# Kernel optimization log

Measured on AMD Instinct MI355X. Metric: run time of the kernel, lower is better.

## Reference

```python
import jax, jax.numpy as jnp
import numpy as np

NUM_USERS = 1000000
NUM_ITEMS = 500000
NUM_R = 5
D = 64
B = 512
N = 30


def _mlp3(x, W1, b1, W2, b2, W3, b3):
    # Linear->ReLU->Linear->ReLU->Linear (as in MLP module)
    h = jax.nn.relu(x @ W1 + b1)
    h = jax.nn.relu(h @ W2 + b2)
    return h @ W3 + b3


def _attn(self_rep, neighs, W1, b1, W2, b2):
    # pi_rep = self_rep.unsqueeze(1).expand_as(neighs)
    rep = jnp.broadcast_to(jnp.expand_dims(self_rep, 1), neighs.shape)
    h = jax.nn.relu(jnp.concatenate([rep, neighs], -1) @ W1 + b1)
    s = h @ W2 + b2
    # NOTE: original torch code uses F.softmax(..., dim=0) (over the batch axis); kept faithfully
    return jax.nn.softmax(s, axis=0)


def _forward(fl, nodes_u, nodes_i, u_items_list, u_users_list, i_users_list,
             u_items_r, u_users_items, u_users_items_r, i_users_r):
    (E_u, E_i, E_r,
     gv_W1, gv_b1, gv_W2, gv_b2, gv_W3, gv_b3,
     attI_W1, attI_b1, attI_W2, attI_b2,
     attO_W1, attO_b1, attO_W2, attO_b2,
     attS_W1, attS_b1, attS_W2, attS_b2,
     atti_W1, atti_b1, atti_W2, atti_b2,
     linI_W, linI_b, linO_W, linO_b,
     umlp_W1, umlp_b1, umlp_W2, umlp_b2, umlp_W3, umlp_b3,
     gu_W1, gu_b1, gu_W2, gu_b2, gu_W3, gu_b3,
     ilin_W, ilin_b,
     g_W1, g_b1, g_W2, g_b2, g_W3, g_b3) = fl

    # ----- UserModeling: item-space aggregation -----
    pi = E_u[nodes_u]                                   # [B, d]
    er = E_r[u_items_r]                                 # [B, N, d]
    qa = E_i[u_items_list]                              # [B, N, d]
    xia = _mlp3(jnp.concatenate([qa, er], -1), gv_W1, gv_b1, gv_W2, gv_b2, gv_W3, gv_b3)
    alpha_ia = _attn(pi, xia, attI_W1, attI_b1, attI_W2, attI_b2)   # [B, N, 1]
    hi_I = jax.nn.relu(jnp.sum(alpha_ia * xia, 1) @ linI_W + linI_b)  # [B, d]

    # ----- UserModeling: social-space aggregation -----
    po = E_u[u_users_list]                              # [B, N, d]
    ero = E_r[u_users_items_r]                          # [B, N, N, d]
    qao = E_i[u_users_items]                            # [B, N, N, d]
    xoa = _mlp3(jnp.concatenate([qao, ero], -1), gv_W1, gv_b1, gv_W2, gv_b2, gv_W3, gv_b3)
    alpha_oa = _attn(po, xoa, attO_W1, attO_b1, attO_W2, attO_b2)   # [B, N, N, 1]
    ho_I = jax.nn.relu(jnp.sum(alpha_oa * xoa, 1) @ linO_W + linO_b)  # [B, N, d]
    # original att_S(ho_I, pi) does not shape-check; intended semantics: pi is self, ho_I are neighbors
    beta_io = _attn(pi, ho_I, attS_W1, attS_b1, attS_W2, attS_b2)   # [B, N, 1]
    hi_S = jax.nn.relu(jnp.sum(beta_io * ho_I, 1) @ linO_W + linO_b)  # original reuses linO (linS unused)
    hi = _mlp3(jnp.concatenate([hi_I, hi_S], -1), umlp_W1, umlp_b1, umlp_W2, umlp_b2, umlp_W3, umlp_b3)

    # ----- ItemModeling -----
    qj = E_i[nodes_i]                                   # [B, d]
    pt = E_u[i_users_list]                              # [B, N, d]
    er2 = E_r[i_users_r]                                # [B, N, d]
    fjt = _mlp3(jnp.concatenate([pt, er2], -1), gu_W1, gu_b1, gu_W2, gu_b2, gu_W3, gu_b3)
    mu_jt = _attn(qj, fjt, atti_W1, atti_b1, atti_W2, atti_b2)      # [B, N, 1]
    zj = jax.nn.relu(jnp.sum(mu_jt * fjt, 1) @ ilin_W + ilin_b)     # [B, d]

    # ----- Rating prediction -----
    gl = _mlp3(jnp.concatenate([hi, zj], -1), g_W1, g_b1, g_W2, g_b2, g_W3, g_b3)  # [B, 1]
    return gl


def setup_inputs() -> dict:
    key = jax.random.key(0)
    ks = iter(jax.random.split(key, 80))
    def P(*shape):
        return jax.random.normal(next(ks), shape, jnp.float32) * 0.05
    def I(shape, hi):
        return jax.random.randint(next(ks), shape, 0, hi, dtype=jnp.int32)
    d = D
    inp = {}
    inp['E_u'] = P(NUM_USERS, d)
    inp['E_i'] = P(NUM_ITEMS, d)
    inp['E_r'] = P(NUM_R, d)
    for pre in ['gv', 'umlp', 'gu']:
        inp[pre + '_W1'] = P(2 * d, d); inp[pre + '_b1'] = P(d)
        inp[pre + '_W2'] = P(d, d);     inp[pre + '_b2'] = P(d)
        inp[pre + '_W3'] = P(d, d);     inp[pre + '_b3'] = P(d)
    for pre in ['attI', 'attO', 'attS', 'atti']:
        inp[pre + '_W1'] = P(2 * d, d); inp[pre + '_b1'] = P(d)
        inp[pre + '_W2'] = P(d, 1);     inp[pre + '_b2'] = P(1)
    inp['linI_W'] = P(d, d); inp['linI_b'] = P(d)
    inp['linO_W'] = P(d, d); inp['linO_b'] = P(d)
    inp['ilin_W'] = P(d, d); inp['ilin_b'] = P(d)
    inp['g_W1'] = P(2 * d, 1); inp['g_b1'] = P(1)
    inp['g_W2'] = P(1, 1);     inp['g_b2'] = P(1)
    inp['g_W3'] = P(1, 1);     inp['g_b3'] = P(1)
    inp['nodes_u'] = I((B,), NUM_USERS)
    inp['nodes_i'] = I((B,), NUM_ITEMS)
    inp['u_items_list'] = I((B, N), NUM_ITEMS)
    inp['u_users_list'] = I((B, N), NUM_USERS)
    inp['i_users_list'] = I((B, N), NUM_USERS)
    inp['u_items_r'] = I((B, N), NUM_R)
    inp['u_users_items'] = I((B, N, N), NUM_ITEMS)
    inp['u_users_items_r'] = I((B, N, N), NUM_R)
    inp['i_users_r'] = I((B, N), NUM_R)
    return inp


def reference(E_u, E_i, E_r,
              gv_W1, gv_b1, gv_W2, gv_b2, gv_W3, gv_b3,
              attI_W1, attI_b1, attI_W2, attI_b2,
              attO_W1, attO_b1, attO_W2, attO_b2,
              attS_W1, attS_b1, attS_W2, attS_b2,
              atti_W1, atti_b1, atti_W2, atti_b2,
              linI_W, linI_b, linO_W, linO_b,
              umlp_W1, umlp_b1, umlp_W2, umlp_b2, umlp_W3, umlp_b3,
              gu_W1, gu_b1, gu_W2, gu_b2, gu_W3, gu_b3,
              ilin_W, ilin_b,
              g_W1, g_b1, g_W2, g_b2, g_W3, g_b3,
              nodes_u, nodes_i, u_items_list, u_users_list, i_users_list,
              u_items_r, u_users_items, u_users_items_r, i_users_r):
    fl = (E_u, E_i, E_r,
          gv_W1, gv_b1, gv_W2, gv_b2, gv_W3, gv_b3,
          attI_W1, attI_b1, attI_W2, attI_b2,
          attO_W1, attO_b1, attO_W2, attO_b2,
          attS_W1, attS_b1, attS_W2, attS_b2,
          atti_W1, atti_b1, atti_W2, atti_b2,
          linI_W, linI_b, linO_W, linO_b,
          umlp_W1, umlp_b1, umlp_W2, umlp_b2, umlp_W3, umlp_b3,
          gu_W1, gu_b1, gu_W2, gu_b2, gu_W3, gu_b3,
          ilin_W, ilin_b,
          g_W1, g_b1, g_W2, g_b2, g_W3, g_b3)
    return _forward(fl, nodes_u, nodes_i, u_items_list, u_users_list, i_users_list,
                    u_items_r, u_users_items, u_users_items_r, i_users_r)
```

## Files before the change

### kernel.cpp

```cpp
#include <hip/hip_runtime.h>
#include <cstdint>
#include <cstddef>


#define GB 512
#define GN 30
#define GD 64
#define IDX16(l) ((((l) & 15) << 2) | ((l) >> 4))

typedef unsigned short u16;
typedef __attribute__((ext_vector_type(8))) short short8v;
typedef __attribute__((ext_vector_type(4))) float f32x4;

__device__ __forceinline__ u16 f2bf(float x) {
  union { float f; uint32_t u; } c; c.f = x;
  uint32_t r = c.u + 0x7fffu + ((c.u >> 16) & 1u);
  return (u16)(r >> 16);
}
__device__ __forceinline__ float bf2f(u16 b) {
  union { float f; uint32_t u; } c; c.u = ((uint32_t)b) << 16; return c.f;
}
__device__ __forceinline__ float wave_sum(float v) {
#pragma unroll
  for (int off = 32; off >= 1; off >>= 1) v += __shfl_xor(v, off, 64);
  return v;
}

__global__ __launch_bounds__(256) void k_setup(
    const float* __restrict__ gvW1, const float* __restrict__ gvW2, const float* __restrict__ gvW3,
    const float* __restrict__ guW1, const float* __restrict__ guW2, const float* __restrict__ guW3,
    const float* __restrict__ umW1, const float* __restrict__ umW2, const float* __restrict__ umW3,
    const float* __restrict__ aOW1, const float* __restrict__ aIW1, const float* __restrict__ aiW1,
    const float* __restrict__ aSW1,
    const float* __restrict__ E_u, const float* __restrict__ E_i,
    const int* __restrict__ nodes_u, const int* __restrict__ nodes_i, const int* __restrict__ u_users,
    u16* gv1t, u16* gv2t, u16* gv3t, u16* gu1t, u16* gu2t, u16* gu3t,
    u16* um1t, u16* um2t, u16* um3t, u16* aOt, u16* aIt, u16* ait,
    float* piWI, float* piWS, float* qjWi, float* poW) {
  __shared__ float ws[64 * 64];
  int blk = blockIdx.x, t = threadIdx.x;
  if (blk < 240) {
    int o = blk * 256 + t;
    const float* src; u16* dst; int kind;
    if      (o < 8192)  {            src = gvW1; dst = gv1t; kind = 0; }
    else if (o < 12288) { o -= 8192;  src = gvW2; dst = gv2t; kind = 1; }
    else if (o < 16384) { o -= 12288; src = gvW3; dst = gv3t; kind = 1; }
    else if (o < 20480) { o -= 16384; src = aOW1; dst = aOt;  kind = 2; }
    else if (o < 28672) { o -= 20480; src = guW1; dst = gu1t; kind = 0; }
    else if (o < 32768) { o -= 28672; src = guW2; dst = gu2t; kind = 1; }
    else if (o < 36864) { o -= 32768; src = guW3; dst = gu3t; kind = 1; }
    else if (o < 40960) { o -= 36864; src = aIW1; dst = aIt;  kind = 2; }
    else if (o < 45056) { o -= 40960; src = aiW1; dst = ait;  kind = 2; }
    else if (o < 53248) { o -= 45056; src = umW1; dst = um1t; kind = 0; }
    else if (o < 57344) { o -= 53248; src = umW2; dst = um2t; kind = 1; }
    else                { o -= 57344; src = umW3; dst = um3t; kind = 1; }
    if (kind == 0) { int n = o >> 7, k = o & 127; dst[n * 128 + k] = f2bf(src[(size_t)k * 64 + n]); }
    else { int n = o >> 6, p = o & 63; int k = ((p & 3) << 4) | (p >> 2); if (kind == 2) k += 64;
           dst[n * 64 + p] = f2bf(src[(size_t)k * 64 + n]); }
    return;
  }
  int rb = blk - 240;
  const float* tab; const int* idx; const float* W; float* out; int base;
  if (rb < 16)      { tab = E_u; idx = nodes_u; W = aIW1; out = piWI; base = rb * 32; }
  else if (rb < 32) { tab = E_u; idx = nodes_u; W = aSW1; out = piWS; base = (rb - 16) * 32; }
  else if (rb < 48) { tab = E_i; idx = nodes_i; W = aiW1; out = qjWi; base = (rb - 32) * 32; }
  else              { tab = E_u; idx = u_users; W = aOW1; out = poW;  base = (rb - 48) * 32; }
  for (int i = t; i < 4096; i += 256) ws[i] = W[i];
  __syncthreads();
  int lane = t & 63, wave = t >> 6;
  int b0 = base + wave * 8;
  const float* p[8]; float acc[8];
#pragma unroll
  for (int r = 0; r < 8; r++) {
    p[r] = tab + (size_t)__builtin_amdgcn_readfirstlane(idx[b0 + r]) * 64;
    acc[r] = 0.f;
  }
#pragma unroll 8
  for (int k = 0; k < 64; k++) {
    float w = ws[k * 64 + lane];
#pragma unroll
    for (int r = 0; r < 8; r++) acc[r] = fmaf(p[r][k], w, acc[r]);
  }
#pragma unroll
  for (int r = 0; r < 8; r++) out[(size_t)(b0 + r) * 64 + lane] = acc[r];
}

__global__ __launch_bounds__(256, 2) void k_engine(
    const float* __restrict__ E_i, const float* __restrict__ E_r, const float* __restrict__ E_u,
    const int* __restrict__ uu_items, const int* __restrict__ uu_items_r,
    const int* __restrict__ u_items, const int* __restrict__ u_items_r,
    const int* __restrict__ i_users, const int* __restrict__ i_users_r,
    const u16* __restrict__ gv1t, const u16* __restrict__ gv2t, const u16* __restrict__ gv3t,
    const u16* __restrict__ gu1t, const u16* __restrict__ gu2t, const u16* __restrict__ gu3t,
    const float* __restrict__ gvb1, const float* __restrict__ gvb2, const float* __restrict__ gvb3,
    const float* __restrict__ gub1, const float* __restrict__ gub2, const float* __restrict__ gub3,
    const u16* __restrict__ aOt, const u16* __restrict__ aIt, const u16* __restrict__ ait,
    const float* __restrict__ aOb1, const float* __restrict__ aIb1, const float* __restrict__ aib1,
    const float* __restrict__ aOW2, const float* __restrict__ aIW2, const float* __restrict__ aiW2,
    const float* __restrict__ aOb2, const float* __restrict__ aIb2, const float* __restrict__ aib2,
    const float* __restrict__ poW, const float* __restrict__ piWI, const float* __restrict__ qjWi,
    u16* __restrict__ xoa_bf, u16* __restrict__ xia_bf, u16* __restrict__ fjt_bf,
    float* __restrict__ sOT, float* __restrict__ sIT, float* __restrict__ siT) {
  __shared__ __align__(16) u16 xs[64 * 136], w1s[64 * 136], hs[64 * 72];
  __shared__ float b1s[64], b2s[64], b3s[64], ab1s[64], aw2s[64];
  int t = threadIdx.x, blk = blockIdx.x;
  const float *tabA, *tabB, *selfW, *b1, *b2, *b3, *ab1, *aW2, *ab2p;
  const int *idxA, *idxB; const u16 *w1t, *w2t, *w3t, *att;
  u16* outB; float* sT; int tile0, modeNN;
  if (blk < 480) {
    tabA = E_i; idxA = uu_items; tabB = E_r; idxB = uu_items_r;
    w1t = gv1t; w2t = gv2t; w3t = gv3t; b1 = gvb1; b2 = gvb2; b3 = gvb3;
    att = aOt; ab1 = aOb1; aW2 = aOW2; ab2p = aOb2; selfW = poW;
    outB = xoa_bf; sT = sOT; tile0 = blk * 15; modeNN = 1;
  } else if (blk < 496) {
    int lb = blk - 480;
    tabA = E_i; idxA = u_items; tabB = E_r; idxB = u_items_r;
    w1t = gv1t; w2t = gv2t; w3t = gv3t; b1 = gvb1; b2 = gvb2; b3 = gvb3;
    att = aIt; ab1 = aIb1; aW2 = aIW2; ab2p = aIb2; selfW = piWI;
    outB = xia_bf; sT = sIT; tile0 = lb * 15; modeNN = 0;
  } else {
    int lb = blk - 496;
    tabA = E_u; idxA = i_users; tabB = E_r; idxB = i_users_r;
    w1t = gu1t; w2t = gu2t; w3t = gu3t; b1 = gub1; b2 = gub2; b3 = gub3;
    att = ait; ab1 = aib1; aW2 = aiW2; ab2p = aib2; selfW = qjWi;
    outB = fjt_bf; sT = siT; tile0 = lb * 15; modeNN = 0;
  }
  const int nt = 15;
  for (int i = t; i < 64 * 16; i += 256) { int n = i >> 4, j = i & 15;
    ((uint4*)(w1s + n * 136))[j] = ((const uint4*)(w1t + n * 128))[j]; }
  if (t < 64) { b1s[t] = b1[t]; b2s[t] = b2[t]; b3s[t] = b3[t];
                ab1s[t] = ab1[t]; aw2s[t] = aW2[t]; }
  __syncthreads();
  const int lane = t & 63, wave = t >> 6, m = lane & 15, quad = lane >> 4;
  const int lr = t >> 2, q = t & 3;
  short8v w2f[8], w3f[8], waf[8];
#pragma unroll
  for (int c = 0; c < 4; c++)
#pragma unroll
    for (int kk = 0; kk < 2; kk++) {
      int off = (c * 16 + m) * 64 + kk * 32 + quad * 8;
      w2f[c * 2 + kk] = *(const short8v*)(w2t + off);
      w3f[c * 2 + kk] = *(const short8v*)(w3t + off);
      waf[c * 2 + kk] = *(const short8v*)(att + off);
    }
  const float ab2v = ab2p[0];
  const f32x4 zz = {0.f, 0.f, 0.f, 0.f};
  float4 fr[8];
  {
    int row = tile0 * 64 + lr;
    const float* src = (q < 2) ? (tabA + (size_t)idxA[row] * 64 + q * 32)
                               : (tabB + (size_t)idxB[row] * 64 + (q - 2) * 32);
#pragma unroll
    for (int h = 0; h < 8; h++) fr[h] = ((const float4*)src)[h];
  }
  for (int it = 0; it < nt; it++) {
    int base = (tile0 + it) * 64;
    { u16* dst = xs + lr * 136 + q * 32;
#pragma unroll
      for (int h = 0; h < 8; h++) { float4 v = fr[h]; ushort4 u;
        u.x = f2bf(v.x); u.y = f2bf(v.y); u.z = f2bf(v.z); u.w = f2bf(v.w);
        *(ushort4*)(dst + h * 4) = u; } }
    if (it + 1 < nt) {
      int row = base + 64 + lr;
      const float* src = (q < 2) ? (tabA + (size_t)idxA[row] * 64 + q * 32)
                                 : (tabB + (size_t)idxB[row] * 64 + (q - 2) * 32);
#pragma unroll
      for (int h = 0; h < 8; h++) fr[h] = ((const float4*)src)[h];
    }
    f32x4 cc[4];
#pragma unroll
    for (int c = 0; c < 4; c++) cc[c] = zz;
#pragma unroll
    for (int kk = 0; kk < 4; kk++) {
      short8v av = *(const short8v*)(xs + (wave * 16 + m) * 136 + kk * 32 + quad * 8);
#pragma unroll
      for (int c = 0; c < 4; c++) {
        short8v bv = *(const short8v*)(w1s + (c * 16 + m) * 136 + kk * 32 + quad * 8);
        cc[c] = __builtin_amdgcn_mfma_f32_16x16x32_bf16(av, bv, cc[c], 0, 0, 0);
      }
    }
#pragma unroll
    for (int r = 0; r < 4; r++) { ushort4 u;
      u.x = f2bf(fmaxf(cc[0][r] + b1s[m], 0.f));
      u.y = f2bf(fmaxf(cc[1][r] + b1s[16 + m], 0.f));
      u.z = f2bf(fmaxf(cc[2][r] + b1s[32 + m], 0.f));
      u.w = f2bf(fmaxf(cc[3][r] + b1s[48 + m], 0.f));
      *(ushort4*)(hs + (wave * 16 + quad * 4 + r) * 72 + m * 4) = u; }
#pragma unroll
    for (int c = 0; c < 4; c++) cc[c] = zz;
#pragma unroll
    for (int kk = 0; kk < 2; kk++) {
      short8v av = *(const short8v*)(hs + (wave * 16 + m) * 72 + kk * 32 + quad * 8);
#pragma unroll
      for (int c = 0; c < 4; c++)
        cc[c] = __builtin_amdgcn_mfma_f32_16x16x32_bf16(av, w2f[c * 2 + kk], cc[c], 0, 0, 0);
    }
#pragma unroll
    for (int r = 0; r < 4; r++) { ushort4 u;
      u.x = f2bf(fmaxf(cc[0][r] + b2s[m], 0.f));
      u.y = f2bf(fmaxf(cc[1][r] + b2s[16 + m], 0.f));
      u.z = f2bf(fmaxf(cc[2][r] + b2s[32 + m], 0.f));
      u.w = f2bf(fmaxf(cc[3][r] + b2s[48 + m], 0.f));
      *(ushort4*)(hs + (wave * 16 + quad * 4 + r) * 72 + m * 4) = u; }
    f32x4 c3[4];
#pragma unroll
    for (int c = 0; c < 4; c++) c3[c] = zz;
#pragma unroll
    for (int kk = 0; kk < 2; kk++) {
      short8v av = *(const short8v*)(hs + (wave * 16 + m) * 72 + kk * 32 + quad * 8);
#pragma unroll
      for (int c = 0; c < 4; c++)
        c3[c] = __builtin_amdgcn_mfma_f32_16x16x32_bf16(av, w3f[c * 2 + kk], c3[c], 0, 0, 0);
    }
#pragma unroll
    for (int r = 0; r < 4; r++) { ushort4 u;
      u.x = f2bf(c3[0][r] + b3s[m]);
      u.y = f2bf(c3[1][r] + b3s[16 + m]);
      u.z = f2bf(c3[2][r] + b3s[32 + m]);
      u.w = f2bf(c3[3][r] + b3s[48 + m]);
      *(ushort4*)(hs + (wave * 16 + quad * 4 + r) * 72 + m * 4) = u; }
#pragma unroll
    for (int c2 = 0; c2 < 2; c2++) {
      int chunk = lane * 2 + c2; int row = chunk >> 3, k8 = chunk & 7;
      *(uint4*)(outB + ((size_t)(base + wave * 16 + row)) * 64 + k8 * 8) =
          *(const uint4*)(hs + (wave * 16 + row) * 72 + k8 * 8);
    }
    f32x4 c4[4];
#pragma unroll
    for (int c = 0; c < 4; c++) c4[c] = zz;
#pragma unroll
    for (int kk = 0; kk < 2; kk++) {
      short8v av = *(const short8v*)(hs + (wave * 16 + m) * 72 + kk * 32 + quad * 8);
#pragma unroll
      for (int c = 0; c < 4; c++)
        c4[c] = __builtin_amdgcn_mfma_f32_16x16x32_bf16(av, waf[c * 2 + kk], c4[c], 0, 0, 0);
    }
    float part[4];
#pragma unroll
    for (int r = 0; r < 4; r++) {
      int gRow = base + wave * 16 + quad * 4 + r;
      int sidx = modeNN ? ((gRow / (GN * GN)) * GN + gRow % GN) : (gRow / GN);
      const float* pw = selfW + (size_t)sidx * 64;
      float s = 0.f;
#pragma unroll
      for (int c = 0; c < 4; c++) {
        int col = c * 16 + m;
        s += fmaxf(c4[c][r] + pw[col] + ab1s[col], 0.f) * aw2s[col];
      }
      part[r] = s;
    }
#pragma unroll
    for (int r = 0; r < 4; r++) {
      float v = part[r];
      v += __shfl_xor(v, 1, 64); v += __shfl_xor(v, 2, 64);
      v += __shfl_xor(v, 4, 64); v += __shfl_xor(v, 8, 64);
      if (m == 0) {
        int gRow = base + wave * 16 + quad * 4 + r;
        int scol, sb;
        if (modeNN) { sb = gRow / (GN * GN); scol = gRow % (GN * GN); }
        else        { sb = gRow / GN;        scol = gRow % GN; }
        sT[(size_t)scol * GB + sb] = v + ab2v;
      }
    }
  }
}

__global__ __launch_bounds__(256) void k_softmax_t(
    float* __restrict__ sIT, float* __restrict__ siT, float* __restrict__ sOT) {
  int blk = blockIdx.x, t = threadIdx.x;
  float* p;
  if (blk < 30)      p = sIT + (size_t)blk * GB;
  else if (blk < 60) p = siT + (size_t)(blk - 30) * GB;
  else               p = sOT + (size_t)(blk - 60) * GB;
  int lane = t & 63, wave = t >> 6;
  float v0 = p[t], v1 = p[t + 256];
  float mx = fmaxf(v0, v1);
#pragma unroll
  for (int off = 32; off >= 1; off >>= 1) mx = fmaxf(mx, __shfl_xor(mx, off, 64));
  __shared__ float rm[4], rs[4];
  if (lane == 0) rm[wave] = mx;
  __syncthreads();
  float M4 = fmaxf(fmaxf(rm[0], rm[1]), fmaxf(rm[2], rm[3]));
  float e0 = expf(v0 - M4), e1 = expf(v1 - M4);
  float sm = wave_sum(e0 + e1);
  if (lane == 0) rs[wave] = sm;
  __syncthreads();
  float inv = 1.f / (rs[0] + rs[1] + rs[2] + rs[3]);
  p[t] = e0 * inv;
  p[t + 256] = e1 * inv;
}

__global__ __launch_bounds__(256) void k_agg(
    const u16* __restrict__ xia_bf, const u16* __restrict__ fjt_bf, const u16* __restrict__ xoa_bf,
    const float* __restrict__ sIT, const float* __restrict__ siT, const float* __restrict__ sOT,
    const float* __restrict__ linIW, const float* __restrict__ linIb,
    const float* __restrict__ ilinW, const float* __restrict__ ilinb,
    const float* __restrict__ linOW, const float* __restrict__ linOb,
    float* __restrict__ hiI, float* __restrict__ zj, float* __restrict__ ho) {
  __shared__ float ws[64 * 64];
  __shared__ float ts[4][64];
  int blk = blockIdx.x, t = threadIdx.x, lane = t & 63, wave = t >> 6;
  const float* W; const float* bias;
  if (blk < 128)      { W = linIW; bias = linIb; }
  else if (blk < 256) { W = ilinW; bias = ilinb; }
  else                { W = linOW; bias = linOb; }
  for (int i = t; i < 4096; i += 256) ws[i] = W[i];
  __syncthreads();
  int px = IDX16(lane);
  float acc = 0.f;
  float* outp;
  if (blk < 256) {
    int b = (blk & 127) * 4 + wave;
    const u16* X = (blk < 128) ? xia_bf : fjt_bf;
    const float* al = (blk < 128) ? sIT : siT;
    for (int n = 0; n < GN; n++)
      acc = fmaf(al[(size_t)n * GB + b], bf2f(X[((size_t)b * GN + n) * 64 + px]), acc);
    outp = ((blk < 128) ? hiI : zj) + (size_t)b * 64;
  } else {
    int gid = (blk - 256) * 4 + wave;
    int b_ = gid / GN, n2 = gid - b_ * GN;
    for (int n1 = 0; n1 < GN; n1++)
      acc = fmaf(sOT[((size_t)(n1 * GN + n2)) * GB + b_],
                 bf2f(xoa_bf[(((size_t)b_ * GN + n1) * GN + n2) * 64 + px]), acc);
    outp = ho + (size_t)gid * 64;
  }
  ts[wave][lane] = acc;
  float o = bias[lane];
#pragma unroll 8
  for (int k = 0; k < 64; k++) o = fmaf(ts[wave][k], ws[k * 64 + lane], o);
  outp[lane] = fmaxf(o, 0.f);
}

__global__ __launch_bounds__(256, 4) void k_score_sS(
    const float* __restrict__ selfW, const float* __restrict__ X,
    const float* __restrict__ W1b, const float* __restrict__ b1,
    const float* __restrict__ W2, const float* __restrict__ b2,
    float* __restrict__ sT) {
  __shared__ float ws[64 * 64];
  __shared__ float w2s[64], b1s[64];
  for (int i = threadIdx.x; i < 64 * 64; i += 256) ws[i] = W1b[i];
  if (threadIdx.x < 64) { w2s[threadIdx.x] = W2[threadIdx.x]; b1s[threadIdx.x] = b1[threadIdx.x]; }
  __syncthreads();
  const int lane = threadIdx.x & 63, wave = threadIdx.x >> 6;
  int rb = (blockIdx.x * 4 + wave) * 8;
  const float* px[8]; float acc[8];
#pragma unroll
  for (int r = 0; r < 8; r++) {
    int row = rb + r;
    px[r] = X + (size_t)row * 64;
    acc[r] = b1s[lane] + selfW[(size_t)(row / GN) * 64 + lane];
  }
#pragma unroll 8
  for (int k = 0; k < 64; k++) {
    float w = ws[k * 64 + lane];
#pragma unroll
    for (int r = 0; r < 8; r++) acc[r] = fmaf(px[r][k], w, acc[r]);
  }
  float bb2 = b2[0];
#pragma unroll
  for (int r = 0; r < 8; r++) {
    float v = fmaxf(acc[r], 0.f) * w2s[lane];
    v = wave_sum(v);
    int row = rb + r;
    if (lane == 0) sT[(size_t)(row % GN) * GB + row / GN] = v + bb2;
  }
}

__global__ __launch_bounds__(256) void k_wsum_hiS(
    const float* __restrict__ ho, const float* __restrict__ sST,
    const float* __restrict__ linOW, const float* __restrict__ linOb,
    float* __restrict__ hiS) {
  __shared__ float ws[64 * 64];
  __shared__ float ts[4][64];
  int t = threadIdx.x, lane = t & 63, wave = t >> 6;
  for (int i = t; i < 4096; i += 256) ws[i] = linOW[i];
  __syncthreads();
  int b = blockIdx.x * 4 + wave;
  float acc = 0.f;
  for (int n = 0; n < GN; n++)
    acc = fmaf(sST[(size_t)n * GB + b], ho[((size_t)b * GN + n) * 64 + lane], acc);
  ts[wave][lane] = acc;
  float o = linOb[lane];
#pragma unroll 8
  for (int k = 0; k < 64; k++) o = fmaf(ts[wave][k], ws[k * 64 + lane], o);
  hiS[(size_t)b * 64 + lane] = fmaxf(o, 0.f);
}

__global__ __launch_bounds__(256, 2) void k_tail(
    const float* __restrict__ hiI, const float* __restrict__ hiS, const float* __restrict__ zj,
    const u16* __restrict__ um1t, const u16* __restrict__ um2t, const u16* __restrict__ um3t,
    const float* __restrict__ umb1, const float* __restrict__ umb2, const float* __restrict__ umb3,
    const float* __restrict__ gW1, const float* __restrict__ gb1,
    const float* __restrict__ gW2, const float* __restrict__ gb2,
    const float* __restrict__ gW3, const float* __restrict__ gb3,
    float* __restrict__ out) {
  __shared__ __align__(16) u16 xs[64 * 136], w1s[64 * 136], hs[64 * 72];
  __shared__ float b1s[64], b2s[64], b3s[64], g1s[128];
  int t = threadIdx.x;
  for (int i = t; i < 64 * 16; i += 256) { int n = i >> 4, j = i & 15;
    ((uint4*)(w1s + n * 136))[j] = ((const uint4*)(um1t + n * 128))[j]; }
  if (t < 64) { b1s[t] = umb1[t]; b2s[t] = umb2[t]; b3s[t] = umb3[t]; }
  if (t < 128) g1s[t] = gW1[t];
  int base = blockIdx.x * 64;
  { int lr = t >> 2, q = t & 3; int b = base + lr;
    const float* src = (q < 2) ? (hiI + (size_t)b * 64 + q * 32)
                               : (hiS + (size_t)b * 64 + (q - 2) * 32);
    u16* dst = xs + lr * 136 + q * 32;
#pragma unroll
    for (int h = 0; h < 8; h++) { float4 v = ((const float4*)src)[h]; ushort4 u;
      u.x = f2bf(v.x); u.y = f2bf(v.y); u.z = f2bf(v.z); u.w = f2bf(v.w);
      *(ushort4*)(dst + h * 4) = u; } }
  __syncthreads();
  const int lane = t & 63, wave = t >> 6, m = lane & 15, quad = lane >> 4;
  short8v w2f[8], w3f[8];
#pragma unroll
  for (int c = 0; c < 4; c++)
#pragma unroll
    for (int kk = 0; kk < 2; kk++) {
      int off = (c * 16 + m) * 64 + kk * 32 + quad * 8;
      w2f[c * 2 + kk] = *(const short8v*)(um2t + off);
      w3f[c * 2 + kk] = *(const short8v*)(um3t + off);
    }
  const f32x4 zz = {0.f, 0.f, 0.f, 0.f};
  f32x4 cc[4];
#pragma unroll
  for (int c = 0; c < 4; c++) cc[c] = zz;
#pragma unroll
  for (int kk = 0; kk < 4; kk++) {
    short8v av = *(const short8v*)(xs + (wave * 16 + m) * 136 + kk * 32 + quad * 8);
#pragma unroll
    for (int c = 0; c < 4; c++) {
      short8v bv = *(const short8v*)(w1s + (c * 16 + m) * 136 + kk * 32 + quad * 8);
      cc[c] = __builtin_amdgcn_mfma_f32_16x16x32_bf16(av, bv, cc[c], 0, 0, 0);
    }
  }
#pragma unroll
  for (int r = 0; r < 4; r++) { ushort4 u;
    u.x = f2bf(fmaxf(cc[0][r] + b1s[m], 0.f));
    u.y = f2bf(fmaxf(cc[1][r] + b1s[16 + m], 0.f));
    u.z = f2bf(fmaxf(cc[2][r] + b1s[32 + m], 0.f));
    u.w = f2bf(fmaxf(cc[3][r] + b1s[48 + m], 0.f));
    *(ushort4*)(hs + (wave * 16 + quad * 4 + r) * 72 + m * 4) = u; }
#pragma unroll
  for (int c = 0; c < 4; c++) cc[c] = zz;
#pragma unroll
  for (int kk = 0; kk < 2; kk++) {
    short8v av = *(const short8v*)(hs + (wave * 16 + m) * 72 + kk * 32 + quad * 8);
#pragma unroll
    for (int c = 0; c < 4; c++)
      cc[c] = __builtin_amdgcn_mfma_f32_16x16x32_bf16(av, w2f[c * 2 + kk], cc[c], 0, 0, 0);
  }
#pragma unroll
  for (int r = 0; r < 4; r++) { ushort4 u;
    u.x = f2bf(fmaxf(cc[0][r] + b2s[m], 0.f));
    u.y = f2bf(fmaxf(cc[1][r] + b2s[16 + m], 0.f));
    u.z = f2bf(fmaxf(cc[2][r] + b2s[32 + m], 0.f));
    u.w = f2bf(fmaxf(cc[3][r] + b2s[48 + m], 0.f));
    *(ushort4*)(hs + (wave * 16 + quad * 4 + r) * 72 + m * 4) = u; }
  f32x4 c3[4];
#pragma unroll
  for (int c = 0; c < 4; c++) c3[c] = zz;
#pragma unroll
  for (int kk = 0; kk < 2; kk++) {
    short8v av = *(const short8v*)(hs + (wave * 16 + m) * 72 + kk * 32 + quad * 8);
#pragma unroll
    for (int c = 0; c < 4; c++)
      c3[c] = __builtin_amdgcn_mfma_f32_16x16x32_bf16(av, w3f[c * 2 + kk], c3[c], 0, 0, 0);
  }
#pragma unroll
  for (int r = 0; r < 4; r++) { ushort4 u;
    u.x = f2bf(c3[0][r] + b3s[m]);
    u.y = f2bf(c3[1][r] + b3s[16 + m]);
    u.z = f2bf(c3[2][r] + b3s[32 + m]);
    u.w = f2bf(c3[3][r] + b3s[48 + m]);
    *(ushort4*)(hs + (wave * 16 + quad * 4 + r) * 72 + m * 4) = u; }
  float gb1v = gb1[0], gb2v = gb2[0], gb3v = gb3[0], gW2v = gW2[0], gW3v = gW3[0];
  int px = IDX16(lane);
  for (int r16 = 0; r16 < 16; r16++) {
    int row = wave * 16 + r16, b = base + row;
    float v = bf2f(hs[row * 72 + px]) * g1s[lane] + zj[(size_t)b * 64 + lane] * g1s[64 + lane];
    v = wave_sum(v);
    if (lane == 0) {
      float h = fmaxf(v + gb1v, 0.f);
      h = fmaxf(h * gW2v + gb2v, 0.f);
      out[b] = h * gW3v + gb3v;
    }
  }
}

extern "C" void kernel_launch(void* const* d_in, const int* in_sizes, int n_in,
                              void* d_out, int out_size, void* d_ws, size_t ws_size,
                              hipStream_t stream) {
  const float* E_u = (const float*)d_in[0];
  const float* E_i = (const float*)d_in[1];
  const float* E_r = (const float*)d_in[2];
  const float* gvW1 = (const float*)d_in[3];  const float* gvb1 = (const float*)d_in[4];
  const float* gvW2 = (const float*)d_in[5];  const float* gvb2 = (const float*)d_in[6];
  const float* gvW3 = (const float*)d_in[7];  const float* gvb3 = (const float*)d_in[8];
  const float* umW1 = (const float*)d_in[9];  const float* umb1 = (const float*)d_in[10];
  const float* umW2 = (const float*)d_in[11]; const float* umb2 = (const float*)d_in[12];
  const float* umW3 = (const float*)d_in[13]; const float* umb3 = (const float*)d_in[14];
  const float* guW1 = (const float*)d_in[15]; const float* gub1 = (const float*)d_in[16];
  const float* guW2 = (const float*)d_in[17]; const float* gub2 = (const float*)d_in[18];
  const float* guW3 = (const float*)d_in[19]; const float* gub3 = (const float*)d_in[20];
  const float* aIW1 = (const float*)d_in[21]; const float* aIb1 = (const float*)d_in[22];
  const float* aIW2 = (const float*)d_in[23]; const float* aIb2 = (const float*)d_in[24];
  const float* aOW1 = (const float*)d_in[25]; const float* aOb1 = (const float*)d_in[26];
  const float* aOW2 = (const float*)d_in[27]; const float* aOb2 = (const float*)d_in[28];
  const float* aSW1 = (const float*)d_in[29]; const float* aSb1 = (const float*)d_in[30];
  const float* aSW2 = (const float*)d_in[31]; const float* aSb2 = (const float*)d_in[32];
  const float* aiW1 = (const float*)d_in[33]; const float* aib1 = (const float*)d_in[34];
  const float* aiW2 = (const float*)d_in[35]; const float* aib2 = (const float*)d_in[36];
  const float* linIW = (const float*)d_in[37]; const float* linIb = (const float*)d_in[38];
  const float* linOW = (const float*)d_in[39]; const float* linOb = (const float*)d_in[40];
  const float* ilinW = (const float*)d_in[41]; const float* ilinb = (const float*)d_in[42];
  const float* gW1 = (const float*)d_in[43]; const float* gb1 = (const float*)d_in[44];
  const float* gW2 = (const float*)d_in[45]; const float* gb2 = (const float*)d_in[46];
  const float* gW3 = (const float*)d_in[47]; const float* gb3 = (const float*)d_in[48];
  const int* nodes_u = (const int*)d_in[49];
  const int* nodes_i = (const int*)d_in[50];
  const int* u_items = (const int*)d_in[51];
  const int* u_users = (const int*)d_in[52];
  const int* i_users = (const int*)d_in[53];
  const int* u_items_r = (const int*)d_in[54];
  const int* uu_items = (const int*)d_in[55];
  const int* uu_items_r = (const int*)d_in[56];
  const int* i_users_r = (const int*)d_in[57];
  float* out = (float*)d_out;

  const int BN = GB * GN;
  const int M2 = GB * GN * GN;

  float* p = (float*)d_ws;
  float* piWI = p; p += GB * GD;
  float* piWS = p; p += GB * GD;
  float* qjWi = p; p += GB * GD;
  float* poW  = p; p += BN * GD;
  float* ho   = p; p += BN * GD;
  float* sIT  = p; p += BN;
  float* siT  = p; p += BN;
  float* sST  = p; p += BN;
  float* sOT  = p; p += M2;
  float* hiI  = p; p += GB * GD;
  float* hiS  = p; p += GB * GD;
  float* zj   = p; p += GB * GD;
  u16* q16 = (u16*)p;
  u16* gv1t = q16; q16 += 8192;
  u16* gv2t = q16; q16 += 4096;
  u16* gv3t = q16; q16 += 4096;
  u16* gu1t = q16; q16 += 8192;
  u16* gu2t = q16; q16 += 4096;
  u16* gu3t = q16; q16 += 4096;
  u16* um1t = q16; q16 += 8192;
  u16* um2t = q16; q16 += 4096;
  u16* um3t = q16; q16 += 4096;
  u16* aOt  = q16; q16 += 4096;
  u16* aIt  = q16; q16 += 4096;
  u16* ait  = q16; q16 += 4096;
  u16* xia_bf = q16; q16 += (size_t)BN * GD;
  u16* fjt_bf = q16; q16 += (size_t)BN * GD;
  u16* xoa_bf = q16; q16 += (size_t)M2 * GD;

  k_setup<<<768, 256, 0, stream>>>(gvW1, gvW2, gvW3, guW1, guW2, guW3,
                                   umW1, umW2, umW3, aOW1, aIW1, aiW1, aSW1,
                                   E_u, E_i, nodes_u, nodes_i, u_users,
                                   gv1t, gv2t, gv3t, gu1t, gu2t, gu3t,
                                   um1t, um2t, um3t, aOt, aIt, ait,
                                   piWI, piWS, qjWi, poW);
  k_engine<<<512, 256, 0, stream>>>(E_i, E_r, E_u,
                                    uu_items, uu_items_r, u_items, u_items_r,
                                    i_users, i_users_r,
                                    gv1t, gv2t, gv3t, gu1t, gu2t, gu3t,
                                    gvb1, gvb2, gvb3, gub1, gub2, gub3,
                                    aOt, aIt, ait, aOb1, aIb1, aib1,
                                    aOW2, aIW2, aiW2, aOb2, aIb2, aib2,
                                    poW, piWI, qjWi,
                                    xoa_bf, xia_bf, fjt_bf, sOT, sIT, siT);
  k_softmax_t<<<960, 256, 0, stream>>>(sIT, siT, sOT);
  k_agg<<<256 + BN / 4, 256, 0, stream>>>(xia_bf, fjt_bf, xoa_bf, sIT, siT, sOT,
                                          linIW, linIb, ilinW, ilinb, linOW, linOb,
                                          hiI, zj, ho);
  k_score_sS<<<BN / 32, 256, 0, stream>>>(piWS, ho, aSW1 + 64 * 64, aSb1, aSW2, aSb2, sST);
  k_softmax_t<<<30, 256, 0, stream>>>(sST, sST, sST);
  k_wsum_hiS<<<GB / 4, 256, 0, stream>>>(ho, sST, linOW, linOb, hiS);
  k_tail<<<GB / 64, 256, 0, stream>>>(hiI, hiS, zj, um1t, um2t, um3t,
                                      umb1, umb2, umb3,
                                      gW1, gb1, gW2, gb2, gW3, gb3, out);
}
```

Baseline: 616.5 us.

## Fuse softmax into aggregation, merge score and tail kernels, restructure gather pipeline

Replaces the in-place softmax kernels with a stats-only pass (max and inverse sum per column), so aggregation kernels recompute normalized weights on the fly instead of re-reading written probabilities. The social attention score computation is fused into k_agg, and the final softmax plus weighted-sum for hiS are folded into k_tail, which removes three launches. In k_engine the attention weights move from registers to LDS, and the gather prefetch now holds only the next row's index rather than a full row of data, which lowers register pressure. The tail now runs the sST softmax and hiS aggregation on only 8 blocks, which risks serializing that work.

```diff
diff --git a/kernel.cpp b/kernel.cpp
--- a/kernel.cpp
+++ b/kernel.cpp
@@ -23,6 +23,11 @@
 __device__ __forceinline__ float wave_sum(float v) {
 #pragma unroll
   for (int off = 32; off >= 1; off >>= 1) v += __shfl_xor(v, off, 64);
+  return v;
+}
+__device__ __forceinline__ float wave_max(float v) {
+#pragma unroll
+  for (int off = 32; off >= 1; off >>= 1) v = fmaxf(v, __shfl_xor(v, off, 64));
   return v;
 }
 
@@ -101,7 +106,7 @@
     const float* __restrict__ poW, const float* __restrict__ piWI, const float* __restrict__ qjWi,
     u16* __restrict__ xoa_bf, u16* __restrict__ xia_bf, u16* __restrict__ fjt_bf,
     float* __restrict__ sOT, float* __restrict__ sIT, float* __restrict__ siT) {
-  __shared__ __align__(16) u16 xs[64 * 136], w1s[64 * 136], hs[64 * 72];
+  __shared__ __align__(16) u16 xs[64 * 136], w1s[64 * 136], was[64 * 72], hs[64 * 72];
   __shared__ float b1s[64], b2s[64], b3s[64], ab1s[64], aw2s[64];
   int t = threadIdx.x, blk = blockIdx.x;
   const float *tabA, *tabB, *selfW, *b1, *b2, *b3, *ab1, *aW2, *ab2p;
@@ -128,12 +133,14 @@
   const int nt = 15;
   for (int i = t; i < 64 * 16; i += 256) { int n = i >> 4, j = i & 15;
     ((uint4*)(w1s + n * 136))[j] = ((const uint4*)(w1t + n * 128))[j]; }
+  for (int i = t; i < 64 * 8; i += 256) { int n = i >> 3, j = i & 7;
+    ((uint4*)(was + n * 72))[j] = ((const uint4*)(att + n * 64))[j]; }
   if (t < 64) { b1s[t] = b1[t]; b2s[t] = b2[t]; b3s[t] = b3[t];
                 ab1s[t] = ab1[t]; aw2s[t] = aW2[t]; }
   __syncthreads();
   const int lane = t & 63, wave = t >> 6, m = lane & 15, quad = lane >> 4;
   const int lr = t >> 2, q = t & 3;
-  short8v w2f[8], w3f[8], waf[8];
+  short8v w2f[8], w3f[8];
 #pragma unroll
   for (int c = 0; c < 4; c++)
 #pragma unroll
@@ -141,31 +148,29 @@
       int off = (c * 16 + m) * 64 + kk * 32 + quad * 8;
       w2f[c * 2 + kk] = *(const short8v*)(w2t + off);
       w3f[c * 2 + kk] = *(const short8v*)(w3t + off);
-      waf[c * 2 + kk] = *(const short8v*)(att + off);
     }
   const float ab2v = ab2p[0];
   const f32x4 zz = {0.f, 0.f, 0.f, 0.f};
-  float4 fr[8];
-  {
-    int row = tile0 * 64 + lr;
-    const float* src = (q < 2) ? (tabA + (size_t)idxA[row] * 64 + q * 32)
-                               : (tabB + (size_t)idxB[row] * 64 + (q - 2) * 32);
-#pragma unroll
-    for (int h = 0; h < 8; h++) fr[h] = ((const float4*)src)[h];
-  }
+  const float* srcTab = (q < 2) ? tabA : tabB;
+  const int qoff = (q < 2) ? q * 32 : (q - 2) * 32;
+  int idxcur;
+  { int row0 = tile0 * 64 + lr; idxcur = (q < 2) ? idxA[row0] : idxB[row0]; }
   for (int it = 0; it < nt; it++) {
     int base = (tile0 + it) * 64;
-    { u16* dst = xs + lr * 136 + q * 32;
-#pragma unroll
-      for (int h = 0; h < 8; h++) { float4 v = fr[h]; ushort4 u;
-        u.x = f2bf(v.x); u.y = f2bf(v.y); u.z = f2bf(v.z); u.w = f2bf(v.w);
-        *(ushort4*)(dst + h * 4) = u; } }
-    if (it + 1 < nt) {
-      int row = base + 64 + lr;
-      const float* src = (q < 2) ? (tabA + (size_t)idxA[row] * 64 + q * 32)
-                                 : (tabB + (size_t)idxB[row] * 64 + (q - 2) * 32);
-#pragma unroll
-      for (int h = 0; h < 8; h++) fr[h] = ((const float4*)src)[h];
+    {
+      const float4* s4 = (const float4*)(srcTab + (size_t)idxcur * 64 + qoff);
+      float4 v[8];
+#pragma unroll
+      for (int h = 0; h < 8; h++) v[h] = s4[h];
+      if (it + 1 < nt) {
+        int rown = base + 64 + lr;
+        idxcur = (q < 2) ? idxA[rown] : idxB[rown];
+      }
+      u16* dst = xs + lr * 136 + q * 32;
+#pragma unroll
+      for (int h = 0; h < 8; h++) { ushort4 u;
+        u.x = f2bf(v[h].x); u.y = f2bf(v[h].y); u.z = f2bf(v[h].z); u.w = f2bf(v[h].w);
+        *(ushort4*)(dst + h * 4) = u; }
     }
     f32x4 cc[4];
 #pragma unroll
@@ -232,8 +237,10 @@
     for (int kk = 0; kk < 2; kk++) {
       short8v av = *(const short8v*)(hs + (wave * 16 + m) * 72 + kk * 32 + quad * 8);
 #pragma unroll
-      for (int c = 0; c < 4; c++)
-        c4[c] = __builtin_amdgcn_mfma_f32_16x16x32_bf16(av, waf[c * 2 + kk], c4[c], 0, 0, 0);
+      for (int c = 0; c < 4; c++) {
+        short8v bv = *(const short8v*)(was + (c * 16 + m) * 72 + kk * 32 + quad * 8);
+        c4[c] = __builtin_amdgcn_mfma_f32_16x16x32_bf16(av, bv, c4[c], 0, 0, 0);
+      }
     }
     float part[4];
 #pragma unroll
@@ -265,129 +272,108 @@
   }
 }
 
-__global__ __launch_bounds__(256) void k_softmax_t(
-    float* __restrict__ sIT, float* __restrict__ siT, float* __restrict__ sOT) {
-  int blk = blockIdx.x, t = threadIdx.x;
-  float* p;
-  if (blk < 30)      p = sIT + (size_t)blk * GB;
-  else if (blk < 60) p = siT + (size_t)(blk - 30) * GB;
-  else               p = sOT + (size_t)(blk - 60) * GB;
+__global__ __launch_bounds__(256) void k_stats(
+    const float* __restrict__ sIT, const float* __restrict__ siT, const float* __restrict__ sOT,
+    float* __restrict__ stats) {
+  int c = blockIdx.x, t = threadIdx.x;
+  const float* p;
+  if (c < 30)      p = sIT + (size_t)c * GB;
+  else if (c < 60) p = siT + (size_t)(c - 30) * GB;
+  else             p = sOT + (size_t)(c - 60) * GB;
   int lane = t & 63, wave = t >> 6;
   float v0 = p[t], v1 = p[t + 256];
-  float mx = fmaxf(v0, v1);
-#pragma unroll
-  for (int off = 32; off >= 1; off >>= 1) mx = fmaxf(mx, __shfl_xor(mx, off, 64));
+  float mx = wave_max(fmaxf(v0, v1));
   __shared__ float rm[4], rs[4];
   if (lane == 0) rm[wave] = mx;
   __syncthreads();
   float M4 = fmaxf(fmaxf(rm[0], rm[1]), fmaxf(rm[2], rm[3]));
-  float e0 = expf(v0 - M4), e1 = expf(v1 - M4);
-  float sm = wave_sum(e0 + e1);
+  float sm = wave_sum(__expf(v0 - M4) + __expf(v1 - M4));
   if (lane == 0) rs[wave] = sm;
   __syncthreads();
-  float inv = 1.f / (rs[0] + rs[1] + rs[2] + rs[3]);
-  p[t] = e0 * inv;
-  p[t + 256] = e1 * inv;
+  if (t == 0) {
+    stats[2 * c] = M4;
+    stats[2 * c + 1] = 1.f / (rs[0] + rs[1] + rs[2] + rs[3]);
+  }
 }
 
 __global__ __launch_bounds__(256) void k_agg(
     const u16* __restrict__ xia_bf, const u16* __restrict__ fjt_bf, const u16* __restrict__ xoa_bf,
     const float* __restrict__ sIT, const float* __restrict__ siT, const float* __restrict__ sOT,
+    const float* __restrict__ stats,
     const float* __restrict__ linIW, const float* __restrict__ linIb,
     const float* __restrict__ ilinW, const float* __restrict__ ilinb,
     const float* __restrict__ linOW, const float* __restrict__ linOb,
-    float* __restrict__ hiI, float* __restrict__ zj, float* __restrict__ ho) {
+    const float* __restrict__ aSW1, const float* __restrict__ aSb1,
+    const float* __restrict__ aSW2, const float* __restrict__ aSb2,
+    const float* __restrict__ piWS,
+    float* __restrict__ hiI, float* __restrict__ zj, float* __restrict__ ho,
+    float* __restrict__ sST) {
   __shared__ float ws[64 * 64];
+  __shared__ float ws2[64 * 64];
   __shared__ float ts[4][64];
   int blk = blockIdx.x, t = threadIdx.x, lane = t & 63, wave = t >> 6;
-  const float* W; const float* bias;
-  if (blk < 128)      { W = linIW; bias = linIb; }
-  else if (blk < 256) { W = ilinW; bias = ilinb; }
-  else                { W = linOW; bias = linOb; }
-  for (int i = t; i < 4096; i += 256) ws[i] = W[i];
+  int px = IDX16(lane);
+  if (blk < 64) {
+    const float* W = (blk < 32) ? linIW : ilinW;
+    for (int i = t; i < 4096; i += 256) ws[i] = W[i];
+    __syncthreads();
+    const u16* X = (blk < 32) ? xia_bf : fjt_bf;
+    const float* sRaw = (blk < 32) ? sIT : siT;
+    const float* st = stats + ((blk < 32) ? 0 : 60);
+    const float* bias = (blk < 32) ? linIb : ilinb;
+    float* outp = (blk < 32) ? hiI : zj;
+    int bbase = (blk & 31) * 16 + wave * 4;
+    for (int bs = 0; bs < 4; bs++) {
+      int b = bbase + bs;
+      float acc = 0.f;
+#pragma unroll 6
+      for (int n = 0; n < GN; n++) {
+        float al = __expf(sRaw[(size_t)n * GB + b] - st[2 * n]) * st[2 * n + 1];
+        acc = fmaf(al, bf2f(X[((size_t)b * GN + n) * 64 + px]), acc);
+      }
+      ts[wave][lane] = acc;
+      float o = bias[lane];
+#pragma unroll 8
+      for (int k = 0; k < 64; k++) o = fmaf(ts[wave][k], ws[k * 64 + lane], o);
+      outp[(size_t)b * 64 + lane] = fmaxf(o, 0.f);
+    }
+    return;
+  }
+  for (int i = t; i < 4096; i += 256) { ws[i] = linOW[i]; ws2[i] = aSW1[64 * 64 + i]; }
   __syncthreads();
-  int px = IDX16(lane);
-  float acc = 0.f;
-  float* outp;
-  if (blk < 256) {
-    int b = (blk & 127) * 4 + wave;
-    const u16* X = (blk < 128) ? xia_bf : fjt_bf;
-    const float* al = (blk < 128) ? sIT : siT;
-    for (int n = 0; n < GN; n++)
-      acc = fmaf(al[(size_t)n * GB + b], bf2f(X[((size_t)b * GN + n) * 64 + px]), acc);
-    outp = ((blk < 128) ? hiI : zj) + (size_t)b * 64;
-  } else {
-    int gid = (blk - 256) * 4 + wave;
+  const float* stO = stats + 2 * 60;
+  float aSb2v = aSb2[0];
+  int gbase = (blk - 64) * 8 + wave * 2;
+  for (int g2 = 0; g2 < 2; g2++) {
+    int gid = gbase + g2;
     int b_ = gid / GN, n2 = gid - b_ * GN;
-    for (int n1 = 0; n1 < GN; n1++)
-      acc = fmaf(sOT[((size_t)(n1 * GN + n2)) * GB + b_],
-                 bf2f(xoa_bf[(((size_t)b_ * GN + n1) * GN + n2) * 64 + px]), acc);
-    outp = ho + (size_t)gid * 64;
-  }
-  ts[wave][lane] = acc;
-  float o = bias[lane];
+    float acc = 0.f;
+#pragma unroll 6
+    for (int n1 = 0; n1 < GN; n1++) {
+      int col = n1 * GN + n2;
+      float al = __expf(sOT[(size_t)col * GB + b_] - stO[2 * col]) * stO[2 * col + 1];
+      acc = fmaf(al, bf2f(xoa_bf[(((size_t)b_ * GN + n1) * GN + n2) * 64 + px]), acc);
+    }
+    ts[wave][lane] = acc;
+    float o = linOb[lane];
 #pragma unroll 8
-  for (int k = 0; k < 64; k++) o = fmaf(ts[wave][k], ws[k * 64 + lane], o);
-  outp[lane] = fmaxf(o, 0.f);
-}
-
-__global__ __launch_bounds__(256, 4) void k_score_sS(
-    const float* __restrict__ selfW, const float* __restrict__ X,
-    const float* __restrict__ W1b, const float* __restrict__ b1,
-    const float* __restrict__ W2, const float* __restrict__ b2,
-    float* __restrict__ sT) {
-  __shared__ float ws[64 * 64];
-  __shared__ float w2s[64], b1s[64];
-  for (int i = threadIdx.x; i < 64 * 64; i += 256) ws[i] = W1b[i];
-  if (threadIdx.x < 64) { w2s[threadIdx.x] = W2[threadIdx.x]; b1s[threadIdx.x] = b1[threadIdx.x]; }
-  __syncthreads();
-  const int lane = threadIdx.x & 63, wave = threadIdx.x >> 6;
-  int rb = (blockIdx.x * 4 + wave) * 8;
-  const float* px[8]; float acc[8];
-#pragma unroll
-  for (int r = 0; r < 8; r++) {
-    int row = rb + r;
-    px[r] = X + (size_t)row * 64;
-    acc[r] = b1s[lane] + selfW[(size_t)(row / GN) * 64 + lane];
-  }
+    for (int k = 0; k < 64; k++) o = fmaf(ts[wave][k], ws[k * 64 + lane], o);
+    o = fmaxf(o, 0.f);
+    ho[(size_t)gid * 64 + lane] = o;
+    ts[wave][lane] = o;
+    float h = piWS[(size_t)b_ * 64 + lane] + aSb1[lane];
 #pragma unroll 8
-  for (int k = 0; k < 64; k++) {
-    float w = ws[k * 64 + lane];
-#pragma unroll
-    for (int r = 0; r < 8; r++) acc[r] = fmaf(px[r][k], w, acc[r]);
-  }
-  float bb2 = b2[0];
-#pragma unroll
-  for (int r = 0; r < 8; r++) {
-    float v = fmaxf(acc[r], 0.f) * w2s[lane];
+    for (int k = 0; k < 64; k++) h = fmaf(ts[wave][k], ws2[k * 64 + lane], h);
+    float v = fmaxf(h, 0.f) * aSW2[lane];
     v = wave_sum(v);
-    int row = rb + r;
-    if (lane == 0) sT[(size_t)(row % GN) * GB + row / GN] = v + bb2;
-  }
-}
-
-__global__ __launch_bounds__(256) void k_wsum_hiS(
+    if (lane == 0) sST[(size_t)n2 * GB + b_] = v + aSb2v;
+  }
+}
+
+__global__ __launch_bounds__(256) void k_tail(
+    const float* __restrict__ hiI, const float* __restrict__ zj,
     const float* __restrict__ ho, const float* __restrict__ sST,
     const float* __restrict__ linOW, const float* __restrict__ linOb,
-    float* __restrict__ hiS) {
-  __shared__ float ws[64 * 64];
-  __shared__ float ts[4][64];
-  int t = threadIdx.x, lane = t & 63, wave = t >> 6;
-  for (int i = t; i < 4096; i += 256) ws[i] = linOW[i];
-  __syncthreads();
-  int b = blockIdx.x * 4 + wave;
-  float acc = 0.f;
-  for (int n = 0; n < GN; n++)
-    acc = fmaf(sST[(size_t)n * GB + b], ho[((size_t)b * GN + n) * 64 + lane], acc);
-  ts[wave][lane] = acc;
-  float o = linOb[lane];
-#pragma unroll 8
-  for (int k = 0; k < 64; k++) o = fmaf(ts[wave][k], ws[k * 64 + lane], o);
-  hiS[(size_t)b * 64 + lane] = fmaxf(o, 0.f);
-}
-
-__global__ __launch_bounds__(256, 2) void k_tail(
-    const float* __restrict__ hiI, const float* __restrict__ hiS, const float* __restrict__ zj,
     const u16* __restrict__ um1t, const u16* __restrict__ um2t, const u16* __restrict__ um3t,
     const float* __restrict__ umb1, const float* __restrict__ umb2, const float* __restrict__ umb3,
     const float* __restrict__ gW1, const float* __restrict__ gb1,
@@ -395,23 +381,50 @@
     const float* __restrict__ gW3, const float* __restrict__ gb3,
     float* __restrict__ out) {
   __shared__ __align__(16) u16 xs[64 * 136], w1s[64 * 136], hs[64 * 72];
+  __shared__ float ws[64 * 64];
+  __shared__ float aM[32], aZi[32];
+  __shared__ float ts[4][64];
   __shared__ float b1s[64], b2s[64], b3s[64], g1s[128];
-  int t = threadIdx.x;
+  int t = threadIdx.x, lane = t & 63, wave = t >> 6, m = lane & 15, quad = lane >> 4;
   for (int i = t; i < 64 * 16; i += 256) { int n = i >> 4, j = i & 15;
     ((uint4*)(w1s + n * 136))[j] = ((const uint4*)(um1t + n * 128))[j]; }
+  for (int i = t; i < 4096; i += 256) ws[i] = linOW[i];
   if (t < 64) { b1s[t] = umb1[t]; b2s[t] = umb2[t]; b3s[t] = umb3[t]; }
   if (t < 128) g1s[t] = gW1[t];
+  for (int c8 = 0; c8 < 8; c8++) {
+    int col = wave * 8 + c8;
+    if (col < GN) {
+      float v[8];
+#pragma unroll
+      for (int j = 0; j < 8; j++) v[j] = sST[(size_t)col * GB + j * 64 + lane];
+      float mx = v[0];
+#pragma unroll
+      for (int j = 1; j < 8; j++) mx = fmaxf(mx, v[j]);
+      mx = wave_max(mx);
+      float z = 0.f;
+#pragma unroll
+      for (int j = 0; j < 8; j++) z += __expf(v[j] - mx);
+      z = wave_sum(z);
+      if (lane == 0) { aM[col] = mx; aZi[col] = 1.f / z; }
+    }
+  }
+  __syncthreads();
   int base = blockIdx.x * 64;
-  { int lr = t >> 2, q = t & 3; int b = base + lr;
-    const float* src = (q < 2) ? (hiI + (size_t)b * 64 + q * 32)
-                               : (hiS + (size_t)b * 64 + (q - 2) * 32);
-    u16* dst = xs + lr * 136 + q * 32;
-#pragma unroll
-    for (int h = 0; h < 8; h++) { float4 v = ((const float4*)src)[h]; ushort4 u;
-      u.x = f2bf(v.x); u.y = f2bf(v.y); u.z = f2bf(v.z); u.w = f2bf(v.w);
-      *(ushort4*)(dst + h * 4) = u; } }
-  __syncthreads();
-  const int lane = t & 63, wave = t >> 6, m = lane & 15, quad = lane >> 4;
+  for (int bi = 0; bi < 16; bi++) {
+    int row = wave * 16 + bi, b = base + row;
+    float acc = 0.f;
+#pragma unroll 6
+    for (int n = 0; n < GN; n++) {
+      float al = __expf(sST[(size_t)n * GB + b] - aM[n]) * aZi[n];
+      acc = fmaf(al, ho[((size_t)b * GN + n) * 64 + lane], acc);
+    }
+    ts[wave][lane] = acc;
+    float o = linOb[lane];
+#pragma unroll 8
+    for (int k = 0; k < 64; k++) o = fmaf(ts[wave][k], ws[k * 64 + lane], o);
+    xs[row * 136 + 64 + lane] = f2bf(fmaxf(o, 0.f));
+    xs[row * 136 + lane] = f2bf(hiI[(size_t)b * 64 + lane]);
+  }
   short8v w2f[8], w3f[8];
 #pragma unroll
   for (int c = 0; c < 4; c++)
@@ -542,8 +555,8 @@
   float* sST  = p; p += BN;
   float* sOT  = p; p += M2;
   float* hiI  = p; p += GB * GD;
-  float* hiS  = p; p += GB * GD;
   float* zj   = p; p += GB * GD;
+  float* stats = p; p += 2 * 1020;
   u16* q16 = (u16*)p;
   u16* gv1t = q16; q16 += 8192;
   u16* gv2t = q16; q16 += 4096;
@@ -576,14 +589,12 @@
                                     aOW2, aIW2, aiW2, aOb2, aIb2, aib2,
                                     poW, piWI, qjWi,
                                     xoa_bf, xia_bf, fjt_bf, sOT, sIT, siT);
-  k_softmax_t<<<960, 256, 0, stream>>>(sIT, siT, sOT);
-  k_agg<<<256 + BN / 4, 256, 0, stream>>>(xia_bf, fjt_bf, xoa_bf, sIT, siT, sOT,
-                                          linIW, linIb, ilinW, ilinb, linOW, linOb,
-                                          hiI, zj, ho);
-  k_score_sS<<<BN / 32, 256, 0, stream>>>(piWS, ho, aSW1 + 64 * 64, aSb1, aSW2, aSb2, sST);
-  k_softmax_t<<<30, 256, 0, stream>>>(sST, sST, sST);
-  k_wsum_hiS<<<GB / 4, 256, 0, stream>>>(ho, sST, linOW, linOb, hiS);
-  k_tail<<<GB / 64, 256, 0, stream>>>(hiI, hiS, zj, um1t, um2t, um3t,
-                                      umb1, umb2, umb3,
+  k_stats<<<1020, 256, 0, stream>>>(sIT, siT, sOT, stats);
+  k_agg<<<64 + BN / 8, 256, 0, stream>>>(xia_bf, fjt_bf, xoa_bf, sIT, siT, sOT, stats,
+                                         linIW, linIb, ilinW, ilinb, linOW, linOb,
+                                         aSW1, aSb1, aSW2, aSb2, piWS,
+                                         hiI, zj, ho, sST);
+  k_tail<<<GB / 64, 256, 0, stream>>>(hiI, zj, ho, sST, linOW, linOb,
+                                      um1t, um2t, um3t, umb1, umb2, umb3,
                                       gW1, gb1, gW2, gb2, gW3, gb3, out);
 }
```

Result: slower. 634.8 us (+3.0%).
